# Kernel optimization log

Hardware: AMD Instinct MI355X
Metric: run time of the kernel (lower is better)

The kernel has to match this reference:

```python
import jax, jax.numpy as jnp
import numpy as np

N, E, G = 50000, 800000, 50
H, D = 4, 64            # num_heads, h_dim
HD = H * D              # next_in_feats = 256
NODE_IN = 6 + 20        # node_s + seq embedding
NEG_SLOPE = 0.2


def setup_inputs() -> dict:
    key = jax.random.key(0)
    ks = jax.random.split(key, 16)
    # graph structure: random edges + self loops so every node has in-degree >= 1
    src = jnp.concatenate([jax.random.randint(ks[0], (E - N,), 0, N), jnp.arange(N)]).astype(jnp.int32)
    dst = jnp.concatenate([jax.random.randint(ks[1], (E - N,), 0, N), jnp.arange(N)]).astype(jnp.int32)
    graph_id = (jnp.arange(N) // (N // G)).astype(jnp.int32)  # 50 graphs of 1000 nodes
    s = 0.05
    inp = {
        'seq': jax.random.randint(ks[2], (N,), 0, 20),
        'node_s': jax.random.normal(ks[3], (N, 6), jnp.float32),
        'src': src, 'dst': dst, 'graph_id': graph_id,
        'W_emb': jax.random.normal(ks[4], (20, 20), jnp.float32) * s,
        'W0': jax.random.normal(ks[5], (NODE_IN, HD), jnp.float32) * s,
        'al0': jax.random.normal(ks[6], (H, D), jnp.float32) * s,
        'ar0': jax.random.normal(ks[7], (H, D), jnp.float32) * s,
        'b0': jnp.zeros((HD,), jnp.float32),
        'W1': jax.random.normal(ks[8], (HD, HD), jnp.float32) * s,
        'al1': jax.random.normal(ks[9], (H, D), jnp.float32) * s,
        'ar1': jax.random.normal(ks[10], (H, D), jnp.float32) * s,
        'b1': jnp.zeros((HD,), jnp.float32),
        'W2': jax.random.normal(ks[11], (HD, HD), jnp.float32) * s,
        'al2': jax.random.normal(ks[12], (H, D), jnp.float32) * s,
        'ar2': jax.random.normal(ks[13], (H, D), jnp.float32) * s,
        'b2': jnp.zeros((HD,), jnp.float32),
        'Wd1': jax.random.normal(ks[14], (HD, 512), jnp.float32) * s,
        'bd1': jnp.zeros((512,), jnp.float32),
        'Wd2': jax.random.normal(ks[15], (512, 1), jnp.float32) * s,
        'bd2': jnp.zeros((1,), jnp.float32),
    }
    return inp


def gat_layer(h, W, al, ar, b, src, dst):
    ft = (h @ W).reshape(N, H, D)                    # [N,H,D]
    el = jnp.einsum('nhd,hd->nh', ft, al)            # src-side score
    er = jnp.einsum('nhd,hd->nh', ft, ar)            # dst-side score
    e = jax.nn.leaky_relu(el[src] + er[dst], NEG_SLOPE)  # [E,H]
    m = jax.lax.stop_gradient(jax.ops.segment_max(e, dst, num_segments=N))
    ee = jnp.exp(e - m[dst])
    z = jax.ops.segment_sum(ee, dst, num_segments=N)     # [N,H]
    alpha = ee / z[dst]                                   # edge softmax over dst
    msg = ft[src] * alpha[:, :, None]                     # [E,H,D]
    out = jax.ops.segment_sum(msg, dst, num_segments=N)   # [N,H,D]
    return out.reshape(N, HD) + b


def reference(seq, node_s, src, dst, graph_id, W_emb, W0, al0, ar0, b0,
              W1, al1, ar1, b1, W2, al2, ar2, b2, Wd1, bd1, Wd2, bd2):
    h = jnp.concatenate([W_emb[seq], node_s], axis=1)     # [N,26]
    h = gat_layer(h, W0, al0, ar0, b0, src, dst)
    h = gat_layer(h, W1, al1, ar1, b1, src, dst)
    h = gat_layer(h, W2, al2, ar2, b2, src, dst)
    h = jax.nn.relu(h)                                    # dropout in eval mode = identity
    out = jax.nn.relu(h @ Wd1 + bd1) @ Wd2 + bd2 + 0.5    # [N,1]
    cnt = jax.ops.segment_sum(jnp.ones((N,), out.dtype), graph_id, num_segments=G)
    g_out = jax.ops.segment_sum(out, graph_id, num_segments=G) / cnt[:, None]  # [G,1]
    return out, g_out
```

## Files before the change

kernel.cpp:

```cpp
#include <hip/hip_runtime.h>
#include <hip/hip_bf16.h>
#include <float.h>

#define NN 50000
#define EE 800000
#define GG 50
#define HH 4
#define DD 64
#define HD 256
#define NODE_IN 26
#define NEG_SLOPE 0.2f

typedef __attribute__((ext_vector_type(8))) short short8v;
typedef __attribute__((ext_vector_type(4))) float floatx4;

static __device__ __forceinline__ ushort f2bf(float f) {
    __hip_bfloat16 b = __float2bfloat16(f);
    return *(ushort*)&b;
}

static __device__ __forceinline__ float bf2f(ushort u) {
    return __uint_as_float(((unsigned)u) << 16);
}

static __device__ __forceinline__ float lrelu(float e) {
    return (e >= 0.f) ? e : NEG_SLOPE * e;
}

__global__ void embed_bf16_kernel(const int* __restrict__ seq,
                                  const float* __restrict__ node_s,
                                  const float* __restrict__ W_emb,
                                  ushort* __restrict__ hbf) {
    int idx = blockIdx.x * blockDim.x + threadIdx.x;
    if (idx >= NN * 32) return;
    int n = idx >> 5;
    int j = idx & 31;
    float v = 0.f;
    if (j < 20)      v = W_emb[seq[n] * 20 + j];
    else if (j < 26) v = node_s[n * 6 + (j - 20)];
    hbf[idx] = f2bf(v);
}

__global__ void wtrans_kernel(const float* __restrict__ W,
                              ushort* __restrict__ Wt,
                              int K, int N, int Kp) {
    int idx = blockIdx.x * blockDim.x + threadIdx.x;
    if (idx >= N * Kp) return;
    int n = idx / Kp;
    int k = idx - n * Kp;
    float v = (k < K) ? W[(size_t)k * N + n] : 0.f;
    Wt[idx] = f2bf(v);
}

__global__ __launch_bounds__(256) void gemm_mfma_kernel(
    const ushort* __restrict__ A, const ushort* __restrict__ Bt,
    ushort* __restrict__ Cbf, float* __restrict__ Cf,
    const float* __restrict__ bias,
    const float* __restrict__ al, const float* __restrict__ ar,
    float* __restrict__ el, float* __restrict__ er,
    int M, int N, int Kp, int relu_out) {
    __shared__ ushort As[128][40];
    __shared__ ushort Bs[64][40];

    int tid  = threadIdx.x;
    int wave = tid >> 6;
    int lane = tid & 63;
    int bm = blockIdx.y * 128;
    int bn = blockIdx.x * 64;

    floatx4 acc[2][4];
    #pragma unroll
    for (int i = 0; i < 2; ++i)
        #pragma unroll
        for (int j = 0; j < 4; ++j)
            acc[i][j] = (floatx4){0.f, 0.f, 0.f, 0.f};

    const int lr = lane & 15;
    const int lk = (lane >> 4) * 8;
    const int lq = lane >> 4;

    for (int k0 = 0; k0 < Kp; k0 += 32) {
        #pragma unroll
        for (int p = 0; p < 2; ++p) {
            int idx = p * 256 + tid;
            int r = idx >> 2, kk = (idx & 3) * 8;
            int gr = bm + r;
            short8v v = {};
            if (gr < M) v = *(const short8v*)(A + (size_t)gr * Kp + k0 + kk);
            *(short8v*)(&As[r][kk]) = v;
        }
        {
            int c = tid >> 2, kk = (tid & 3) * 8;
            short8v v = *(const short8v*)(Bt + (size_t)(bn + c) * Kp + k0 + kk);
            *(short8v*)(&Bs[c][kk]) = v;
        }
        __syncthreads();

        short8v bfrag[4];
        #pragma unroll
        for (int cs = 0; cs < 4; ++cs)
            bfrag[cs] = *(const short8v*)(&Bs[cs * 16 + lr][lk]);
        #pragma unroll
        for (int rs = 0; rs < 2; ++rs) {
            short8v afrag = *(const short8v*)(&As[wave * 32 + rs * 16 + lr][lk]);
            #pragma unroll
            for (int cs = 0; cs < 4; ++cs)
                acc[rs][cs] = __builtin_amdgcn_mfma_f32_16x16x32_bf16(
                    afrag, bfrag[cs], acc[rs][cs], 0, 0, 0);
        }
        __syncthreads();
    }

    const int h_blk = bn >> 6;
    float alv[4], arv[4];
    if (al) {
        #pragma unroll
        for (int cs = 0; cs < 4; ++cs) {
            alv[cs] = al[h_blk * DD + cs * 16 + lr];
            arv[cs] = ar[h_blk * DD + cs * 16 + lr];
        }
    }

    #pragma unroll
    for (int rs = 0; rs < 2; ++rs)
        #pragma unroll
        for (int j = 0; j < 4; ++j) {
            int row = bm + wave * 32 + rs * 16 + lq * 4 + j;
            if (row >= M) continue;
            float sl = 0.f, sr = 0.f;
            #pragma unroll
            for (int cs = 0; cs < 4; ++cs) {
                float raw = acc[rs][cs][j];
                float v = raw;
                int col = bn + cs * 16 + lr;
                if (bias) v += bias[col];
                if (relu_out) v = fmaxf(v, 0.f);
                if (Cbf) Cbf[(size_t)row * N + col] = f2bf(v);
                else     Cf [(size_t)row * N + col] = v;
                if (al) {
                    sl = fmaf(raw, alv[cs], sl);
                    sr = fmaf(raw, arv[cs], sr);
                }
            }
            if (al) {
                #pragma unroll
                for (int off = 1; off < 16; off <<= 1) {
                    sl += __shfl_xor(sl, off);
                    sr += __shfl_xor(sr, off);
                }
                if (lr == 0) {
                    el[row * HH + h_blk] = sl;
                    er[row * HH + h_blk] = sr;
                }
            }
        }
}

__global__ void hist_kernel(const int* __restrict__ dst, int* __restrict__ cnt) {
    for (int i = blockIdx.x * blockDim.x + threadIdx.x; i < EE;
         i += gridDim.x * blockDim.x)
        atomicAdd(&cnt[dst[i]], 1);
}

__global__ __launch_bounds__(1024) void scan_kernel(
    const int* __restrict__ cnt, int* __restrict__ rowptr) {
    __shared__ int part[1024];
    int t = threadIdx.x;
    const int per = (NN + 1023) / 1024;
    int start = t * per;
    int end = start + per; if (end > NN) end = NN;
    int s = 0;
    for (int i = start; i < end; ++i) s += cnt[i];
    part[t] = s;
    __syncthreads();
    for (int off = 1; off < 1024; off <<= 1) {
        int v = (t >= off) ? part[t - off] : 0;
        __syncthreads();
        part[t] += v;
        __syncthreads();
    }
    int run = (t == 0) ? 0 : part[t - 1];
    for (int i = start; i < end; ++i) { rowptr[i] = run; run += cnt[i]; }
    if (t == 1023) rowptr[NN] = part[1023];
}

__global__ void scatter_kernel(const int* __restrict__ src,
                               const int* __restrict__ dst,
                               const int* __restrict__ rowptr,
                               int* __restrict__ fill,
                               int* __restrict__ colsrc) {
    for (int i = blockIdx.x * blockDim.x + threadIdx.x; i < EE;
         i += gridDim.x * blockDim.x) {
        int d = dst[i];
        int pos = atomicAdd(&fill[d], 1);
        colsrc[rowptr[d] + pos] = src[i];
    }
}

__global__ __launch_bounds__(256) void aggregate_kernel(
    const ushort* __restrict__ ft, const float* __restrict__ el,
    const float* __restrict__ er, const int* __restrict__ rowptr,
    const int* __restrict__ colsrc, const float* __restrict__ bias,
    ushort* __restrict__ out, int relu_out) {
    __shared__ float4 plds[4][64];
    __shared__ int    slds[4][64];

    int v = (blockIdx.x * blockDim.x + threadIdx.x) >> 6;
    int lane = threadIdx.x & 63;
    int w = threadIdx.x >> 6;
    if (v >= NN) return;
    int base = rowptr[v];
    int deg = rowptr[v + 1] - base;

    const int h = lane >> 4;
    float4 er4 = ((const float4*)er)[v];

    float z0 = 0.f, z1 = 0.f, z2 = 0.f, z3 = 0.f;
    float4 acc = {0.f, 0.f, 0.f, 0.f};
    const float* pf = (const float*)plds[w];

    for (int c = 0; c < deg; c += 64) {
        int clen = min(64, deg - c);
        if (lane < clen) {
            int s_j = colsrc[base + c + lane];
            float4 el4 = ((const float4*)el)[s_j];
            float p0 = expf(lrelu(el4.x + er4.x));
            float p1 = expf(lrelu(el4.y + er4.y));
            float p2 = expf(lrelu(el4.z + er4.z));
            float p3 = expf(lrelu(el4.w + er4.w));
            z0 += p0; z1 += p1; z2 += p2; z3 += p3;
            slds[w][lane] = s_j;
            plds[w][lane] = (float4){p0, p1, p2, p3};
        }
        #pragma unroll 4
        for (int jj = 0; jj < clen; ++jj) {
            int   s = slds[w][jj];
            float q = pf[jj * 4 + h];
            ushort4 f4 = ((const ushort4*)(ft + (size_t)s * HD))[lane];
            acc.x = fmaf(q, bf2f(f4.x), acc.x);
            acc.y = fmaf(q, bf2f(f4.y), acc.y);
            acc.z = fmaf(q, bf2f(f4.z), acc.z);
            acc.w = fmaf(q, bf2f(f4.w), acc.w);
        }
    }

    #pragma unroll
    for (int off = 32; off; off >>= 1) {
        z0 += __shfl_xor(z0, off);
        z1 += __shfl_xor(z1, off);
        z2 += __shfl_xor(z2, off);
        z3 += __shfl_xor(z3, off);
    }
    float zh = (h < 2) ? ((h == 0) ? z0 : z1) : ((h == 2) ? z2 : z3);
    float zi = 1.f / zh;

    float4 b4 = ((const float4*)bias)[lane];
    float o0 = acc.x * zi + b4.x;
    float o1 = acc.y * zi + b4.y;
    float o2 = acc.z * zi + b4.z;
    float o3 = acc.w * zi + b4.w;
    if (relu_out) {
        o0 = fmaxf(o0, 0.f); o1 = fmaxf(o1, 0.f);
        o2 = fmaxf(o2, 0.f); o3 = fmaxf(o3, 0.f);
    }
    ushort4 st = {f2bf(o0), f2bf(o1), f2bf(o2), f2bf(o3)};
    *(ushort4*)(out + (size_t)v * HD + lane * 4) = st;
}

__global__ __launch_bounds__(256) void final_kernel(
    const float* __restrict__ hidden, const float* __restrict__ Wd2,
    const float* __restrict__ bd2, float* __restrict__ out) {
    int n = (blockIdx.x * blockDim.x + threadIdx.x) >> 6;
    int lane = threadIdx.x & 63;
    if (n >= NN) return;
    const float4* hr = (const float4*)(hidden + (size_t)n * 512);
    const float4* w  = (const float4*)Wd2;
    float4 a0 = hr[lane];
    float4 a1 = hr[lane + 64];
    float4 w0 = w[lane];
    float4 w1 = w[lane + 64];
    float s = a0.x * w0.x + a0.y * w0.y + a0.z * w0.z + a0.w * w0.w
            + a1.x * w1.x + a1.y * w1.y + a1.z * w1.z + a1.w * w1.w;
    #pragma unroll
    for (int off = 32; off; off >>= 1) s += __shfl_xor(s, off);
    if (lane == 0) out[n] = s + bd2[0] + 0.5f;
}

__global__ __launch_bounds__(256) void pool_kernel(
    const float* __restrict__ out, const int* __restrict__ graph_id,
    float* __restrict__ gout) {
    int g = blockIdx.x;
    int t = threadIdx.x;
    float s = 0.f;
    float c = 0.f;
    for (int n = t; n < NN; n += 256) {
        if (graph_id[n] == g) { s += out[n]; c += 1.f; }
    }
    __shared__ float ss[256], cc[256];
    ss[t] = s; cc[t] = c;
    __syncthreads();
    for (int off = 128; off; off >>= 1) {
        if (t < off) { ss[t] += ss[t + off]; cc[t] += cc[t + off]; }
        __syncthreads();
    }
    if (t == 0) gout[g] = ss[0] / cc[0];
}

static inline size_t align_up(size_t x, size_t a) { return (x + a - 1) & ~(a - 1); }

extern "C" void kernel_launch(void* const* d_in, const int* in_sizes, int n_in,
                              void* d_out, int out_size, void* d_ws, size_t ws_size,
                              hipStream_t stream) {
    const int*   seq    = (const int*)d_in[0];
    const float* node_s = (const float*)d_in[1];
    const int*   src    = (const int*)d_in[2];
    const int*   dst    = (const int*)d_in[3];
    const int*   graph_id = (const int*)d_in[4];
    const float* W_emb  = (const float*)d_in[5];
    const float* W0     = (const float*)d_in[6];
    const float* al0    = (const float*)d_in[7];
    const float* ar0    = (const float*)d_in[8];
    const float* b0     = (const float*)d_in[9];
    const float* W1     = (const float*)d_in[10];
    const float* al1    = (const float*)d_in[11];
    const float* ar1    = (const float*)d_in[12];
    const float* b1     = (const float*)d_in[13];
    const float* W2     = (const float*)d_in[14];
    const float* al2    = (const float*)d_in[15];
    const float* ar2    = (const float*)d_in[16];
    const float* b2     = (const float*)d_in[17];
    const float* Wd1    = (const float*)d_in[18];
    const float* bd1    = (const float*)d_in[19];
    const float* Wd2    = (const float*)d_in[20];
    const float* bd2    = (const float*)d_in[21];

    float* out_nodes  = (float*)d_out;
    float* out_graphs = (float*)d_out + NN;

    char* p = (char*)d_ws;
    size_t off = 0;
    auto alloc = [&](size_t bytes) {
        void* r = p + off;
        off = align_up(off + bytes, 256);
        return r;
    };
    ushort* ftbf  = (ushort*)alloc((size_t)NN * HD * 2);
    float*  hidden= (float*)alloc((size_t)NN * 512 * 4);
    ushort* hbf0  = (ushort*)alloc((size_t)NN * 32 * 2);
    ushort* hbuf  = (ushort*)alloc((size_t)NN * HD * 2);
    float*  el    = (float*)alloc((size_t)NN * HH * 4);
    float*  er    = (float*)alloc((size_t)NN * HH * 4);
    int*    rowptr= (int*)alloc((size_t)(NN + 1) * 4);
    int*    fill  = (int*)alloc((size_t)NN * 4);
    int*    colsrc= (int*)alloc((size_t)EE * 4);
    ushort* Wt0   = (ushort*)alloc((size_t)HD * 32 * 2);
    ushort* Wt1   = (ushort*)alloc((size_t)HD * HD * 2);
    ushort* Wt2   = (ushort*)alloc((size_t)HD * HD * 2);
    ushort* Wtd1  = (ushort*)alloc((size_t)512 * HD * 2);
    (void)ws_size;

    hipMemsetAsync(fill, 0, (size_t)NN * 4, stream);
    hist_kernel<<<1024, 256, 0, stream>>>(dst, fill);
    scan_kernel<<<1, 1024, 0, stream>>>(fill, rowptr);
    hipMemsetAsync(fill, 0, (size_t)NN * 4, stream);
    scatter_kernel<<<1024, 256, 0, stream>>>(src, dst, rowptr, fill, colsrc);

    wtrans_kernel<<<(HD * 32 + 255) / 256, 256, 0, stream>>>(W0, Wt0, NODE_IN, HD, 32);
    wtrans_kernel<<<(HD * HD + 255) / 256, 256, 0, stream>>>(W1, Wt1, HD, HD, HD);
    wtrans_kernel<<<(HD * HD + 255) / 256, 256, 0, stream>>>(W2, Wt2, HD, HD, HD);
    wtrans_kernel<<<(512 * HD + 255) / 256, 256, 0, stream>>>(Wd1, Wtd1, HD, 512, HD);

    embed_bf16_kernel<<<(NN * 32 + 255) / 256, 256, 0, stream>>>(seq, node_s, W_emb, hbf0);

    const int nodeWaves = (NN * 64 + 255) / 256;
    dim3 gemm256(256 / 64, (NN + 127) / 128);
    dim3 gemm512(512 / 64, (NN + 127) / 128);

    gemm_mfma_kernel<<<gemm256, 256, 0, stream>>>(hbf0, Wt0, ftbf, nullptr, nullptr,
                                                  al0, ar0, el, er, NN, HD, 32, 0);
    aggregate_kernel<<<nodeWaves, 256, 0, stream>>>(ftbf, el, er, rowptr, colsrc, b0, hbuf, 0);

    gemm_mfma_kernel<<<gemm256, 256, 0, stream>>>(hbuf, Wt1, ftbf, nullptr, nullptr,
                                                  al1, ar1, el, er, NN, HD, HD, 0);
    aggregate_kernel<<<nodeWaves, 256, 0, stream>>>(ftbf, el, er, rowptr, colsrc, b1, hbuf, 0);

    gemm_mfma_kernel<<<gemm256, 256, 0, stream>>>(hbuf, Wt2, ftbf, nullptr, nullptr,
                                                  al2, ar2, el, er, NN, HD, HD, 0);
    aggregate_kernel<<<nodeWaves, 256, 0, stream>>>(ftbf, el, er, rowptr, colsrc, b2, hbuf, 1);

    gemm_mfma_kernel<<<gemm512, 256, 0, stream>>>(hbuf, Wtd1, nullptr, hidden, bd1,
                                                  nullptr, nullptr, nullptr, nullptr,
                                                  NN, 512, HD, 1);
    final_kernel<<<nodeWaves, 256, 0, stream>>>(hidden, Wd2, bd2, out_nodes);
    pool_kernel<<<GG, 256, 0, stream>>>(out_nodes, graph_id, out_graphs);
}
```

Measured before the change: 653.4 us.

## Replace single-block prefix scan with multi-block three-pass scan; unroll aggregate loop more

The single 1024-thread scan block, which walked about 49 counts per thread serially, is replaced by a three-kernel reduce/scan-block-sums/final-scan scheme spread over about 196 blocks. This removes a serial single-CU bottleneck in building the CSR row pointers. It adds two extra kernel launches. The inner gather loop in the aggregate kernel is also unrolled by 8 instead of 4, to expose more memory-level parallelism at the cost of register pressure.

```diff
diff --git a/kernel.cpp b/kernel.cpp
--- a/kernel.cpp
+++ b/kernel.cpp
@@ -10,6 +10,7 @@
 #define HD 256
 #define NODE_IN 26
 #define NEG_SLOPE 0.2f
+#define SCAN_NB ((NN + 255) / 256)
 
 typedef __attribute__((ext_vector_type(8))) short short8v;
 typedef __attribute__((ext_vector_type(4))) float floatx4;
@@ -162,26 +163,56 @@
         atomicAdd(&cnt[dst[i]], 1);
 }
 
-__global__ __launch_bounds__(1024) void scan_kernel(
-    const int* __restrict__ cnt, int* __restrict__ rowptr) {
-    __shared__ int part[1024];
+__global__ __launch_bounds__(256) void scan_partial_kernel(
+    const int* __restrict__ cnt, int* __restrict__ bsum) {
+    __shared__ int s[256];
+    int b = blockIdx.x, t = threadIdx.x;
+    int i = b * 256 + t;
+    s[t] = (i < NN) ? cnt[i] : 0;
+    __syncthreads();
+    for (int off = 128; off; off >>= 1) {
+        if (t < off) s[t] += s[t + off];
+        __syncthreads();
+    }
+    if (t == 0) bsum[b] = s[0];
+}
+
+__global__ __launch_bounds__(256) void scan_bsums_kernel(
+    const int* __restrict__ bsum, int* __restrict__ boff) {
+    __shared__ int s[256];
     int t = threadIdx.x;
-    const int per = (NN + 1023) / 1024;
-    int start = t * per;
-    int end = start + per; if (end > NN) end = NN;
-    int s = 0;
-    for (int i = start; i < end; ++i) s += cnt[i];
-    part[t] = s;
+    int v = (t < SCAN_NB) ? bsum[t] : 0;
+    s[t] = v;
     __syncthreads();
-    for (int off = 1; off < 1024; off <<= 1) {
-        int v = (t >= off) ? part[t - off] : 0;
-        __syncthreads();
-        part[t] += v;
-        __syncthreads();
-    }
-    int run = (t == 0) ? 0 : part[t - 1];
-    for (int i = start; i < end; ++i) { rowptr[i] = run; run += cnt[i]; }
-    if (t == 1023) rowptr[NN] = part[1023];
+    #pragma unroll
+    for (int off = 1; off < 256; off <<= 1) {
+        int u = (t >= off) ? s[t - off] : 0;
+        __syncthreads();
+        s[t] += u;
+        __syncthreads();
+    }
+    if (t < SCAN_NB) boff[t] = s[t] - v;
+}
+
+__global__ __launch_bounds__(256) void scan_final_kernel(
+    const int* __restrict__ cnt, const int* __restrict__ boff,
+    int* __restrict__ rowptr) {
+    __shared__ int s[256];
+    int b = blockIdx.x, t = threadIdx.x;
+    int i = b * 256 + t;
+    int v = (i < NN) ? cnt[i] : 0;
+    s[t] = v;
+    __syncthreads();
+    #pragma unroll
+    for (int off = 1; off < 256; off <<= 1) {
+        int u = (t >= off) ? s[t - off] : 0;
+        __syncthreads();
+        s[t] += u;
+        __syncthreads();
+    }
+    int incl = s[t] + boff[b];
+    if (i < NN) rowptr[i] = incl - v;
+    if (i == NN - 1) rowptr[NN] = incl;
 }
 
 __global__ void scatter_kernel(const int* __restrict__ src,
@@ -232,7 +263,7 @@
             slds[w][lane] = s_j;
             plds[w][lane] = (float4){p0, p1, p2, p3};
         }
-        #pragma unroll 4
+        #pragma unroll 8
         for (int jj = 0; jj < clen; ++jj) {
             int   s = slds[w][jj];
             float q = pf[jj * 4 + h];
@@ -353,6 +384,8 @@
     int*    rowptr= (int*)alloc((size_t)(NN + 1) * 4);
     int*    fill  = (int*)alloc((size_t)NN * 4);
     int*    colsrc= (int*)alloc((size_t)EE * 4);
+    int*    bsum  = (int*)alloc(256 * 4);
+    int*    boff  = (int*)alloc(256 * 4);
     ushort* Wt0   = (ushort*)alloc((size_t)HD * 32 * 2);
     ushort* Wt1   = (ushort*)alloc((size_t)HD * HD * 2);
     ushort* Wt2   = (ushort*)alloc((size_t)HD * HD * 2);
@@ -361,7 +394,9 @@
 
     hipMemsetAsync(fill, 0, (size_t)NN * 4, stream);
     hist_kernel<<<1024, 256, 0, stream>>>(dst, fill);
-    scan_kernel<<<1, 1024, 0, stream>>>(fill, rowptr);
+    scan_partial_kernel<<<SCAN_NB, 256, 0, stream>>>(fill, bsum);
+    scan_bsums_kernel<<<1, 256, 0, stream>>>(bsum, boff);
+    scan_final_kernel<<<SCAN_NB, 256, 0, stream>>>(fill, boff, rowptr);
     hipMemsetAsync(fill, 0, (size_t)NN * 4, stream);
     scatter_kernel<<<1024, 256, 0, stream>>>(src, dst, rowptr, fill, colsrc);
 
```

New measurement: 637.0 us. 2.5% less time.
